# Performance work log

Hardware: AMD Instinct MI355X
Metric: run time of the kernel (lower is better)

## Reference

```python
import jax, jax.numpy as jnp
import numpy as np


def _rope(x, pos, theta):
    # x: [b, s, h, d], pos: [s] int. Standard interleaved RoPE on even/odd pairs.
    d = x.shape[-1]
    inv_freq = theta ** (-jnp.arange(0, d, 2, dtype=jnp.float32) / d)  # [d/2]
    ang = pos.astype(jnp.float32)[:, None] * inv_freq                  # [s, d/2]
    cos = jnp.cos(ang)[None, :, None, :]
    sin = jnp.sin(ang)[None, :, None, :]
    x1 = x[..., 0::2]
    x2 = x[..., 1::2]
    rot = jnp.stack([x1 * cos - x2 * sin, x1 * sin + x2 * cos], axis=-1)
    return rot.reshape(x.shape)


def setup_inputs() -> dict:
    key = jax.random.key(0)
    ks = jax.random.split(key, 5)
    b, s, d = 4, 2048, 1024
    scale = 1.0 / np.sqrt(d)
    return {
        "x": jax.random.normal(ks[0], (b, s, d), dtype=jnp.float32),
        "W_Q": jax.random.normal(ks[1], (d, d), dtype=jnp.float32) * scale,
        "W_K": jax.random.normal(ks[2], (d, d), dtype=jnp.float32) * scale,
        "W_V": jax.random.normal(ks[3], (d, d), dtype=jnp.float32) * scale,
        "W_O": jax.random.normal(ks[4], (d, d), dtype=jnp.float32) * scale,
        "token_positions": jnp.arange(s, dtype=jnp.int32),
    }


def reference(x, W_Q, W_K, W_V, W_O, token_positions):
    num_heads = 16
    theta = 10000.0
    b, s, d_model = x.shape
    d_k = d_model // num_heads

    Q = x @ W_Q.T  # [b, s, d_model]
    K = x @ W_K.T
    V = x @ W_V.T

    # split heads: last dim is [h0 | h1 | ...] so reshape to [b, s, h, d_k]
    Qh = Q.reshape(b, s, num_heads, d_k)
    Kh = K.reshape(b, s, num_heads, d_k)
    Vh = V.reshape(b, s, num_heads, d_k)

    Qh = _rope(Qh, token_positions, theta)
    Kh = _rope(Kh, token_positions, theta)

    scores = jnp.einsum("bqhd,bkhd->bhqk", Qh, Kh) / jnp.sqrt(
        jnp.asarray(d_k, dtype=x.dtype)
    )
    causal = jnp.tril(jnp.ones((s, s), dtype=bool))  # True = keep
    scores = jnp.where(causal[None, None, :, :], scores, jnp.asarray(-jnp.inf, x.dtype))
    probs = jax.nn.softmax(scores, axis=-1)

    out = jnp.einsum("bhqk,bkhd->bqhd", probs, Vh).reshape(b, s, d_model)
    return out @ W_O.T
```

## Files before the change

kernel.cpp:

```cpp
#include <hip/hip_runtime.h>
#include <type_traits>

typedef __attribute__((ext_vector_type(8))) short short8;
typedef __attribute__((ext_vector_type(4))) float f32x4;
typedef unsigned short u16;
typedef unsigned int   u32;
typedef unsigned long long u64;


static __device__ __forceinline__ u16 f2b(float f) {
  u32 u = __builtin_bit_cast(u32, f);
  u = (u + 0x7fffu + ((u >> 16) & 1u)) >> 16;
  return (u16)u;
}
static __device__ __forceinline__ float b2f(u16 h) {
  return __builtin_bit_cast(float, ((u32)h) << 16);
}

typedef __attribute__((address_space(1))) const unsigned int gas_u32;
typedef __attribute__((address_space(3))) unsigned int las_u32;
static __device__ __forceinline__ void glds16(const u16* g, u16* l) {
  __builtin_amdgcn_global_load_lds((gas_u32*)g, (las_u32*)l, 16, 0, 0);
}

__global__ __launch_bounds__(256) void cvt_all(
    const float* __restrict__ x, const float* __restrict__ wq,
    const float* __restrict__ wk, const float* __restrict__ wv,
    const float* __restrict__ wo, u16* __restrict__ xb, u16* __restrict__ wqb,
    u16* __restrict__ wkb, u16* __restrict__ wvb, u16* __restrict__ wob) {
  int u = blockIdx.x * 256 + threadIdx.x;
  if (u >= 3145728) return;
  const float* src; u16* dst; int off;
  if (u < 2097152) { src = x; dst = xb; off = u; }
  else {
    int t = u - 2097152;
    int w = t >> 18;
    off = t & 0x3FFFF;
    src = (w == 0) ? wq : (w == 1) ? wk : (w == 2) ? wv : wo;
    dst = (w == 0) ? wqb : (w == 1) ? wkb : (w == 2) ? wvb : wob;
  }
  int i = off * 4;
  float4 v = *(const float4*)(src + i);
  union { u16 us[4]; u64 ull; } o;
  o.us[0] = f2b(v.x); o.us[1] = f2b(v.y); o.us[2] = f2b(v.z); o.us[3] = f2b(v.w);
  *(u64*)(dst + i) = o.ull;
}

template <typename OT>
static __device__ __forceinline__ void gemm_body(const u16* __restrict__ A,
                                                 const u16* __restrict__ B,
                                                 OT* __restrict__ C,
                                                 int m0, int n0) {
  __shared__ u16 As[4096];
  __shared__ u16 Bs[4096];

  const int tid  = threadIdx.x;
  const int lane = tid & 63;
  const int wv   = tid >> 6;
  const int quad = lane >> 4;
  const int cc   = lane & 15;
  const int wr   = wv >> 1;
  const int wc   = wv & 1;

  f32x4 acc[4][4];
#pragma unroll
  for (int i = 0; i < 4; i++)
#pragma unroll
    for (int j = 0; j < 4; j++) acc[i][j] = (f32x4){0.f, 0.f, 0.f, 0.f};

  const int p0 = wv * 128 + lane;
  const int p1 = p0 + 64;
  const int r0 = p0 >> 2, g0 = (p0 & 3) ^ (r0 & 3);
  const int r1 = p1 >> 2, g1 = (p1 & 3) ^ (r1 & 3);
  const u16* gA0 = A + (size_t)(m0 + r0) * 1024 + g0 * 8;
  const u16* gA1 = A + (size_t)(m0 + r1) * 1024 + g1 * 8;
  const u16* gB0 = B + (size_t)(n0 + r0) * 1024 + g0 * 8;
  const u16* gB1 = B + (size_t)(n0 + r1) * 1024 + g1 * 8;
  u16* lA = As + wv * 1024;
  u16* lB = Bs + wv * 1024;

  for (int k0 = 0; k0 < 1024; k0 += 32) {
    __syncthreads();
    glds16(gA0 + k0, lA);
    glds16(gA1 + k0, lA + 512);
    glds16(gB0 + k0, lB);
    glds16(gB1 + k0, lB + 512);
    __syncthreads();

    short8 af[4], bf[4];
#pragma unroll
    for (int mt = 0; mt < 4; mt++) {
      int ra = wr * 64 + mt * 16 + cc;
      af[mt] = *(const short8*)&As[ra * 32 + ((quad ^ (ra & 3)) * 8)];
    }
#pragma unroll
    for (int nt = 0; nt < 4; nt++) {
      int rb = wc * 64 + nt * 16 + cc;
      bf[nt] = *(const short8*)&Bs[rb * 32 + ((quad ^ (rb & 3)) * 8)];
    }
#pragma unroll
    for (int mt = 0; mt < 4; mt++)
#pragma unroll
      for (int nt = 0; nt < 4; nt++)
        acc[mt][nt] = __builtin_amdgcn_mfma_f32_16x16x32_bf16(af[mt], bf[nt], acc[mt][nt], 0, 0, 0);
  }

#pragma unroll
  for (int mt = 0; mt < 4; mt++)
#pragma unroll
    for (int nt = 0; nt < 4; nt++)
#pragma unroll
      for (int r = 0; r < 4; r++) {
        int row = m0 + wr * 64 + mt * 16 + quad * 4 + r;
        int col = n0 + wc * 64 + nt * 16 + cc;
        if constexpr (std::is_same_v<OT, float>)
          C[(size_t)row * 1024 + col] = acc[mt][nt][r];
        else
          C[(size_t)row * 1024 + col] = f2b(acc[mt][nt][r]);
      }
}

__global__ __launch_bounds__(256) void gemm_qkv(const u16* __restrict__ A,
                                                const u16* __restrict__ Bq,
                                                const u16* __restrict__ Bk,
                                                const u16* __restrict__ Bv,
                                                u16* __restrict__ Q,
                                                u16* __restrict__ K,
                                                u16* __restrict__ V) {
  int sel = blockIdx.x >> 3;
  const u16* B = (sel == 0) ? Bq : (sel == 1) ? Bk : Bv;
  u16* C = (sel == 0) ? Q : (sel == 1) ? K : V;
  gemm_body<u16>(A, B, C, blockIdx.y * 128, (blockIdx.x & 7) * 128);
}

__global__ __launch_bounds__(256) void gemm_out(const u16* __restrict__ A,
                                                const u16* __restrict__ B,
                                                float* __restrict__ C) {
  gemm_body<float>(A, B, C, blockIdx.y * 128, blockIdx.x * 128);
}

__global__ __launch_bounds__(256) void rope_kernel(u16* __restrict__ Q,
                                                   u16* __restrict__ K,
                                                   const int* __restrict__ pos) {
  u16* T = blockIdx.y ? K : Q;
  const float sc = blockIdx.y ? 1.0f : 0.125f;
  int idx = blockIdx.x * 256 + threadIdx.x;
  int row = idx >> 9;
  int p   = idx & 511;
  int i   = p & 31;
  int col = (p >> 5) * 64 + 2 * i;
  int s   = row & 2047;
  float ps  = (float)pos[s];
  float inv = exp2f(-(float)i * 0.41524101186092033f);
  float ang = ps * inv;
  float sn, cs;
  sincosf(ang, &sn, &cs);
  u32 v = *(u32*)(T + (size_t)row * 1024 + col);
  float x1 = b2f((u16)(v & 0xffffu));
  float x2 = b2f((u16)(v >> 16));
  float y1 = (x1 * cs - x2 * sn) * sc;
  float y2 = (x1 * sn + x2 * cs) * sc;
  *(u32*)(T + (size_t)row * 1024 + col) = (u32)f2b(y1) | ((u32)f2b(y2) << 16);
}

__global__ __launch_bounds__(256) void transpose_v(const u16* __restrict__ V,
                                                   u16* __restrict__ Vt) {
  __shared__ u16 t[64][65];
  int s0 = blockIdx.x * 64;
  int bh = blockIdx.y;
  int b = bh >> 4, h = bh & 15;
  int tid = threadIdx.x;
  int r = tid >> 2, ch = (tid & 3) * 16;
  const u16* src = V + (size_t)(b * 2048 + s0 + r) * 1024 + h * 64 + ch;
  union { uint4 v[2]; u16 us[16]; } tmp;
  tmp.v[0] = *(const uint4*)src;
  tmp.v[1] = *(const uint4*)(src + 8);
#pragma unroll
  for (int j = 0; j < 16; j++) t[r][ch + j] = tmp.us[j];
  __syncthreads();
  union { uint4 v[2]; u16 us[16]; } o;
#pragma unroll
  for (int j = 0; j < 16; j++) o.us[j] = t[ch + j][r];
  u16* dst = Vt + (size_t)(bh * 64 + r) * 2048 + s0 + ch;
  *(uint4*)dst = o.v[0];
  *(uint4*)(dst + 8) = o.v[1];
}

__global__ __launch_bounds__(256) void attn_kernel(const u16* __restrict__ Q,
                                                   const u16* __restrict__ K,
                                                   const u16* __restrict__ Vt,
                                                   u16* __restrict__ O) {
  __shared__ u16 Ks[128][72];
  __shared__ u16 Vs[64][136];
  __shared__ u16 Ps[4][16][136];

  const int bh = blockIdx.x;
  const int qt = 15 - blockIdx.y;
  const int b = bh >> 4, h = bh & 15;
  const int tid  = threadIdx.x;
  const int lane = tid & 63;
  const int wv   = tid >> 6;
  const int quad = lane >> 4;
  const int cc   = lane & 15;
  const int q0   = qt * 128;

  short8 qf[2][2];
#pragma unroll
  for (int mt = 0; mt < 2; mt++) {
    const u16* qp = Q + (size_t)(b * 2048 + q0 + wv * 32 + mt * 16 + cc) * 1024 + h * 64;
    qf[mt][0] = *(const short8*)(qp + quad * 8);
    qf[mt][1] = *(const short8*)(qp + 32 + quad * 8);
  }

  f32x4 o_acc[2][4];
  float m_i[2] = {-3.0e38f, -3.0e38f}, l_i[2] = {0.f, 0.f};
#pragma unroll
  for (int mt = 0; mt < 2; mt++)
#pragma unroll
    for (int nt = 0; nt < 4; nt++) o_acc[mt][nt] = (f32x4){0.f, 0.f, 0.f, 0.f};

  const int krow = tid >> 1, kc = (tid & 1) * 32;
  const u16* Kg = K + ((size_t)(b * 2048) + krow) * 1024 + h * 64 + kc;
  const int vrow = tid >> 2, vc = (tid & 3) * 32;
  const u16* Vg = Vt + ((size_t)(bh * 64) + vrow) * 2048 + vc;

  const int nkt = qt + 1;
  uint4 kpf[4], vpf[4];
#pragma unroll
  for (int j = 0; j < 4; j++) {
    kpf[j] = *(const uint4*)(Kg + j * 8);
    vpf[j] = *(const uint4*)(Vg + j * 8);
  }

  for (int kt = 0; kt < nkt; ++kt) {
    __syncthreads();
#pragma unroll
    for (int j = 0; j < 4; j++) {
      *(uint4*)&Ks[krow][kc + j * 8] = kpf[j];
      *(uint4*)&Vs[vrow][vc + j * 8] = vpf[j];
    }
    __syncthreads();

    if (kt + 1 < nkt) {
      Kg += 131072;
      Vg += 128;
#pragma unroll
      for (int j = 0; j < 4; j++) {
        kpf[j] = *(const uint4*)(Kg + j * 8);
        vpf[j] = *(const uint4*)(Vg + j * 8);
      }
    }

    const bool diag = (kt == qt);

#pragma unroll
    for (int mt = 0; mt < 2; ++mt) {
      f32x4 s[8];
#pragma unroll
      for (int nt = 0; nt < 8; ++nt) {
        short8 bk0 = *(const short8*)&Ks[nt * 16 + cc][quad * 8];
        short8 bk1 = *(const short8*)&Ks[nt * 16 + cc][32 + quad * 8];
        f32x4 z = (f32x4){0.f, 0.f, 0.f, 0.f};
        z = __builtin_amdgcn_mfma_f32_16x16x32_bf16(bk0, qf[mt][0], z, 0, 0, 0);
        s[nt] = __builtin_amdgcn_mfma_f32_16x16x32_bf16(bk1, qf[mt][1], z, 0, 0, 0);
      }

      const int qg = q0 + wv * 32 + mt * 16 + cc;
      const int kb = kt * 128 + quad * 4;
      float mx = -3.0e38f;
#pragma unroll
      for (int nt = 0; nt < 8; ++nt)
#pragma unroll
        for (int r = 0; r < 4; ++r) {
          if (diag && (kb + nt * 16 + r > qg)) s[nt][r] = -3.0e38f;
          mx = fmaxf(mx, s[nt][r]);
        }
      mx = fmaxf(mx, __shfl_xor(mx, 16));
      mx = fmaxf(mx, __shfl_xor(mx, 32));
      const float mn = fmaxf(m_i[mt], mx);
      const float al = __expf(m_i[mt] - mn);
      m_i[mt] = mn;

      float ps = 0.f;
#pragma unroll
      for (int nt = 0; nt < 8; ++nt) {
        float e0 = __expf(s[nt][0] - mn);
        float e1 = __expf(s[nt][1] - mn);
        float e2 = __expf(s[nt][2] - mn);
        float e3 = __expf(s[nt][3] - mn);
        ps += (e0 + e1) + (e2 + e3);
        u64 pk = (u64)f2b(e0) | ((u64)f2b(e1) << 16) |
                 ((u64)f2b(e2) << 32) | ((u64)f2b(e3) << 48);
        *(u64*)&Ps[wv][cc][nt * 16 + quad * 4] = pk;
      }
      l_i[mt] = l_i[mt] * al + ps;

      f32x4 al4;
#pragma unroll
      for (int r = 0; r < 4; ++r) al4[r] = __shfl(al, quad * 4 + r);
#pragma unroll
      for (int nt = 0; nt < 4; ++nt) o_acc[mt][nt] *= al4;

      short8 pa[4];
#pragma unroll
      for (int ks = 0; ks < 4; ++ks)
        pa[ks] = *(const short8*)&Ps[wv][cc][ks * 32 + quad * 8];

#pragma unroll
      for (int nt = 0; nt < 4; ++nt)
#pragma unroll
        for (int ks = 0; ks < 4; ++ks) {
          short8 bv = *(const short8*)&Vs[nt * 16 + cc][ks * 32 + quad * 8];
          o_acc[mt][nt] = __builtin_amdgcn_mfma_f32_16x16x32_bf16(pa[ks], bv, o_acc[mt][nt], 0, 0, 0);
        }
    }
  }

#pragma unroll
  for (int mt = 0; mt < 2; ++mt) {
    float l = l_i[mt];
    l += __shfl_xor(l, 16);
    l += __shfl_xor(l, 32);
    const float linv = 1.0f / l;
    f32x4 li4;
#pragma unroll
    for (int r = 0; r < 4; ++r) li4[r] = __shfl(linv, quad * 4 + r);
    const int rowb = b * 2048 + q0 + wv * 32 + mt * 16 + quad * 4;
#pragma unroll
    for (int nt = 0; nt < 4; ++nt)
#pragma unroll
      for (int r = 0; r < 4; ++r)
        O[(size_t)(rowb + r) * 1024 + h * 64 + nt * 16 + cc] = f2b(o_acc[mt][nt][r] * li4[r]);
  }
}

extern "C" void kernel_launch(void* const* d_in, const int* in_sizes, int n_in,
                              void* d_out, int out_size, void* d_ws, size_t ws_size,
                              hipStream_t stream) {
  const float* x  = (const float*)d_in[0];
  const float* wq = (const float*)d_in[1];
  const float* wk = (const float*)d_in[2];
  const float* wv = (const float*)d_in[3];
  const float* wo = (const float*)d_in[4];
  const int* pos  = (const int*)d_in[5];
  float* out = (float*)d_out;

  char* ws = (char*)d_ws;
  u16* xb  = (u16*)(ws);
  u16* vt  = (u16*)(ws);
  u16* wqb = (u16*)(ws + (16ull << 20));
  u16* wkb = (u16*)(ws + (18ull << 20));
  u16* wvb = (u16*)(ws + (20ull << 20));
  u16* wob = (u16*)(ws + (22ull << 20));
  u16* Qb  = (u16*)(ws + (24ull << 20));
  u16* Kb  = (u16*)(ws + (40ull << 20));
  u16* Vb  = (u16*)(ws + (56ull << 20));
  u16* aO  = Vb;

  cvt_all<<<12288, 256, 0, stream>>>(x, wq, wk, wv, wo, xb, wqb, wkb, wvb, wob);
  gemm_qkv<<<dim3(24, 64), 256, 0, stream>>>(xb, wqb, wkb, wvb, Qb, Kb, Vb);
  rope_kernel<<<dim3(16384, 2), 256, 0, stream>>>(Qb, Kb, pos);
  transpose_v<<<dim3(32, 64), 256, 0, stream>>>(Vb, vt);
  attn_kernel<<<dim3(64, 16), 256, 0, stream>>>(Qb, Kb, vt, aO);
  gemm_out<<<dim3(8, 64), 256, 0, stream>>>(aO, wob, out);
}
```

Measured before the change: 344.5 us.

## Use direct global-to-LDS loads with swizzled K/V and register-resident P

Replaces the register-prefetched K/V tile copy with global_load_lds direct-to-LDS transfers into XOR/rotation-swizzled unpadded layouts, and adjusts the fragment reads to match. When the 16x16x16 bf16 MFMA is available, the softmax probabilities stay in registers as the A operand, which drops the Ps shared buffer round trip. It also separates the causal masking from the max loop and uses the packed bf16 conversion intrinsic. The software prefetch overlap is lost, since loads now sit between two barriers, and using twice as many smaller MFMAs may cost throughput.

```diff
diff --git a/kernel.cpp b/kernel.cpp
--- a/kernel.cpp
+++ b/kernel.cpp
@@ -1,13 +1,25 @@
 #include <hip/hip_runtime.h>
+#include <hip/hip_bf16.h>
 #include <type_traits>
 
 typedef __attribute__((ext_vector_type(8))) short short8;
+typedef __attribute__((ext_vector_type(4))) short s16x4;
 typedef __attribute__((ext_vector_type(4))) float f32x4;
 typedef unsigned short u16;
 typedef unsigned int   u32;
 typedef unsigned long long u64;
 
 
+#if __has_builtin(__builtin_amdgcn_mfma_f32_16x16x16bf16_1k)
+#define MFMA16(a, b, c) __builtin_amdgcn_mfma_f32_16x16x16bf16_1k(a, b, c, 0, 0, 0)
+#define HAVE_MFMA16 1
+#elif __has_builtin(__builtin_amdgcn_mfma_f32_16x16x16_bf16)
+#define MFMA16(a, b, c) __builtin_amdgcn_mfma_f32_16x16x16_bf16(a, b, c, 0, 0, 0)
+#define HAVE_MFMA16 1
+#else
+#define HAVE_MFMA16 0
+#endif
+
 static __device__ __forceinline__ u16 f2b(float f) {
   u32 u = __builtin_bit_cast(u32, f);
   u = (u + 0x7fffu + ((u >> 16) & 1u)) >> 16;
@@ -15,6 +27,11 @@
 }
 static __device__ __forceinline__ float b2f(u16 h) {
   return __builtin_bit_cast(float, ((u32)h) << 16);
+}
+static __device__ __forceinline__ u32 pkbf(float a, float b) {
+  union { __hip_bfloat162 t; u32 u; } c;
+  c.t = __float22bfloat162_rn(make_float2(a, b));
+  return c.u;
 }
 
 typedef __attribute__((address_space(1))) const unsigned int gas_u32;
@@ -190,9 +207,11 @@
                                                    const u16* __restrict__ K,
                                                    const u16* __restrict__ Vt,
                                                    u16* __restrict__ O) {
-  __shared__ u16 Ks[128][72];
-  __shared__ u16 Vs[64][136];
-  __shared__ u16 Ps[4][16][136];
+  __shared__ u16 Ks[8192];
+  __shared__ u16 Vs[8192];
+#if !HAVE_MFMA16
+  __shared__ u16 Ps[4 * 16 * 136];
+#endif
 
   const int bh = blockIdx.x;
   const int qt = 15 - blockIdx.y;
@@ -219,38 +238,28 @@
 #pragma unroll
     for (int nt = 0; nt < 4; nt++) o_acc[mt][nt] = (f32x4){0.f, 0.f, 0.f, 0.f};
 
-  const int krow = tid >> 1, kc = (tid & 1) * 32;
-  const u16* Kg = K + ((size_t)(b * 2048) + krow) * 1024 + h * 64 + kc;
-  const int vrow = tid >> 2, vc = (tid & 3) * 32;
-  const u16* Vg = Vt + ((size_t)(bh * 64) + vrow) * 2048 + vc;
+  const u16* Kp = K + ((size_t)(b * 2048) + wv * 32 + (lane >> 3)) * 1024 + h * 64 +
+                  (((lane & 7) ^ (lane >> 3)) * 8);
+  const u16* Vp[4];
+#pragma unroll
+  for (int j = 0; j < 4; j++) {
+    int rl = wv * 16 + j * 4 + (lane >> 4);
+    int g  = ((lane & 15) - rl) & 15;
+    Vp[j] = Vt + ((size_t)(bh * 64) + rl) * 2048 + g * 8;
+  }
 
   const int nkt = qt + 1;
-  uint4 kpf[4], vpf[4];
-#pragma unroll
-  for (int j = 0; j < 4; j++) {
-    kpf[j] = *(const uint4*)(Kg + j * 8);
-    vpf[j] = *(const uint4*)(Vg + j * 8);
-  }
+  const int pk0 = (quad ^ (cc & 7)) * 8;
 
   for (int kt = 0; kt < nkt; ++kt) {
     __syncthreads();
 #pragma unroll
     for (int j = 0; j < 4; j++) {
-      *(uint4*)&Ks[krow][kc + j * 8] = kpf[j];
-      *(uint4*)&Vs[vrow][vc + j * 8] = vpf[j];
+      glds16(Kp + (size_t)kt * 131072 + j * 8192, Ks + wv * 2048 + j * 512);
+      glds16(Vp[j] + kt * 128, Vs + wv * 2048 + j * 512);
     }
     __syncthreads();
 
-    if (kt + 1 < nkt) {
-      Kg += 131072;
-      Vg += 128;
-#pragma unroll
-      for (int j = 0; j < 4; j++) {
-        kpf[j] = *(const uint4*)(Kg + j * 8);
-        vpf[j] = *(const uint4*)(Vg + j * 8);
-      }
-    }
-
     const bool diag = (kt == qt);
 
 #pragma unroll
@@ -258,29 +267,36 @@
       f32x4 s[8];
 #pragma unroll
       for (int nt = 0; nt < 8; ++nt) {
-        short8 bk0 = *(const short8*)&Ks[nt * 16 + cc][quad * 8];
-        short8 bk1 = *(const short8*)&Ks[nt * 16 + cc][32 + quad * 8];
+        const int rbase = (nt * 16 + cc) * 64;
+        short8 bk0 = *(const short8*)&Ks[rbase + pk0];
+        short8 bk1 = *(const short8*)&Ks[rbase + (pk0 ^ 32)];
         f32x4 z = (f32x4){0.f, 0.f, 0.f, 0.f};
         z = __builtin_amdgcn_mfma_f32_16x16x32_bf16(bk0, qf[mt][0], z, 0, 0, 0);
         s[nt] = __builtin_amdgcn_mfma_f32_16x16x32_bf16(bk1, qf[mt][1], z, 0, 0, 0);
       }
 
-      const int qg = q0 + wv * 32 + mt * 16 + cc;
-      const int kb = kt * 128 + quad * 4;
-      float mx = -3.0e38f;
+      if (diag) {
+        const int qg = q0 + wv * 32 + mt * 16 + cc;
+        const int kb = kt * 128 + quad * 4;
+#pragma unroll
+        for (int nt = 0; nt < 8; ++nt)
+#pragma unroll
+          for (int r = 0; r < 4; ++r)
+            if (kb + nt * 16 + r > qg) s[nt][r] = -3.0e38f;
+      }
+
+      float mx = s[0][0];
 #pragma unroll
       for (int nt = 0; nt < 8; ++nt)
 #pragma unroll
-        for (int r = 0; r < 4; ++r) {
-          if (diag && (kb + nt * 16 + r > qg)) s[nt][r] = -3.0e38f;
-          mx = fmaxf(mx, s[nt][r]);
-        }
+        for (int r = 0; r < 4; ++r) mx = fmaxf(mx, s[nt][r]);
       mx = fmaxf(mx, __shfl_xor(mx, 16));
       mx = fmaxf(mx, __shfl_xor(mx, 32));
       const float mn = fmaxf(m_i[mt], mx);
       const float al = __expf(m_i[mt] - mn);
       m_i[mt] = mn;
 
+      s16x4 pf[8];
       float ps = 0.f;
 #pragma unroll
       for (int nt = 0; nt < 8; ++nt) {
@@ -289,9 +305,10 @@
         float e2 = __expf(s[nt][2] - mn);
         float e3 = __expf(s[nt][3] - mn);
         ps += (e0 + e1) + (e2 + e3);
-        u64 pk = (u64)f2b(e0) | ((u64)f2b(e1) << 16) |
-                 ((u64)f2b(e2) << 32) | ((u64)f2b(e3) << 48);
-        *(u64*)&Ps[wv][cc][nt * 16 + quad * 4] = pk;
+        union { u32 w[2]; s16x4 v; } pu;
+        pu.w[0] = pkbf(e0, e1);
+        pu.w[1] = pkbf(e2, e3);
+        pf[nt] = pu.v;
       }
       l_i[mt] = l_i[mt] * al + ps;
 
@@ -301,18 +318,38 @@
 #pragma unroll
       for (int nt = 0; nt < 4; ++nt) o_acc[mt][nt] *= al4;
 
+#if HAVE_MFMA16
+#pragma unroll
+      for (int nt = 0; nt < 4; ++nt) {
+        const int rv = (nt * 16 + cc) * 128;
+#pragma unroll
+        for (int kk = 0; kk < 8; ++kk) {
+          const int pos = (kk * 2 + (quad >> 1) + cc) & 15;
+          s16x4 bv = *(const s16x4*)&Vs[rv + pos * 8 + (quad & 1) * 4];
+          o_acc[mt][nt] = MFMA16(pf[kk], bv, o_acc[mt][nt]);
+        }
+      }
+#else
+#pragma unroll
+      for (int nt = 0; nt < 8; ++nt) {
+        union { s16x4 v; u64 ull; } pu2; pu2.v = pf[nt];
+        *(u64*)&Ps[(wv * 16 + cc) * 136 + nt * 16 + quad * 4] = pu2.ull;
+      }
       short8 pa[4];
 #pragma unroll
       for (int ks = 0; ks < 4; ++ks)
-        pa[ks] = *(const short8*)&Ps[wv][cc][ks * 32 + quad * 8];
-
-#pragma unroll
-      for (int nt = 0; nt < 4; ++nt)
+        pa[ks] = *(const short8*)&Ps[(wv * 16 + cc) * 136 + ks * 32 + quad * 8];
+#pragma unroll
+      for (int nt = 0; nt < 4; ++nt) {
+        const int rv = (nt * 16 + cc) * 128;
 #pragma unroll
         for (int ks = 0; ks < 4; ++ks) {
-          short8 bv = *(const short8*)&Vs[nt * 16 + cc][ks * 32 + quad * 8];
+          const int pos = (ks * 4 + quad + cc) & 15;
+          short8 bv = *(const short8*)&Vs[rv + pos * 8];
           o_acc[mt][nt] = __builtin_amdgcn_mfma_f32_16x16x32_bf16(pa[ks], bv, o_acc[mt][nt], 0, 0, 0);
         }
+      }
+#endif
     }
   }
 
```

Measured after the change: 299.0 us. 1.15x faster.
